# Kernel optimization log

Measured on AMD Instinct MI355X. Metric: run time of the kernel, lower is better.

Reference implementation:

```python
import jax, jax.numpy as jnp
import numpy as np

R_MAX = 6.0
P = 6.0
QQ = 14.399645 * 0.5  # metal units, * 0.5


def setup_inputs() -> dict:
    key = jax.random.key(0)
    k1, k2, k3, k4 = jax.random.split(key, 4)
    n_atoms = 100_000
    n_edges = 6_400_000
    num_types = 4
    # atomic numbers for H, C, O, Cu
    Z = jnp.asarray([1.0, 6.0, 8.0, 29.0], dtype=jnp.float32)
    # edge lengths in (0.1, 7.3) so some edges exceed r_max and get cut off
    r = jax.random.uniform(k1, (n_edges,), dtype=jnp.float32) * 7.2 + 0.1
    per_atom_energy = jax.random.normal(k2, (n_atoms, 1), dtype=jnp.float32)
    atom_types = jax.random.randint(k3, (n_atoms,), 0, num_types, dtype=jnp.int64)
    edge_index = jax.random.randint(k4, (2, n_edges), 0, n_atoms, dtype=jnp.int64)
    return {"Z": Z, "r": r, "per_atom_energy": per_atom_energy,
            "atom_types": atom_types, "edge_index": edge_index}


def _zbl_edge_energy(Z, r, atom_types, edge_index):
    pzbl = 0.23
    a0 = 0.4685
    c1, c2, c3, c4 = 0.02817, 0.28022, 0.50986, 0.18175
    d1, d2, d3, d4 = -0.20162, -0.4029, -0.94229, -3.1998
    edge_types = atom_types[edge_index]          # (2, E)
    Zpair = Z[edge_types]                        # (2, E)
    Zi, Zj = Zpair[0], Zpair[1]
    x = (jnp.power(Zi, pzbl) + jnp.power(Zj, pzbl)) * r / a0
    psi = (c1 * jnp.exp(d1 * x) + c2 * jnp.exp(d2 * x)
           + c3 * jnp.exp(d3 * x) + c4 * jnp.exp(d4 * x))
    eng = QQ * (Zi * Zj / r) * psi
    rr = r / R_MAX
    p = P
    cutoff = (1.0 - (p + 1.0) * (p + 2.0) / 2.0 * jnp.power(rr, p)
              + p * (p + 2.0) * jnp.power(rr, p + 1.0)
              - p * (p + 1.0) / 2.0 * jnp.power(rr, p + 2.0))
    cutoff = cutoff * (rr < 1.0).astype(cutoff.dtype)
    return cutoff * eng                          # (E,)


def reference(Z, r, per_atom_energy, atom_types, edge_index):
    edge_eng = _zbl_edge_energy(Z, r, atom_types, edge_index)
    n_atoms = per_atom_energy.shape[0]
    atomic_eng = jax.ops.segment_sum(edge_eng, edge_index[0],
                                     num_segments=n_atoms)[:, None]
    return atomic_eng + per_atom_energy
```

## Files before the change

kernel.cpp:

```cpp
#include <hip/hip_runtime.h>


namespace {
constexpr float PZBL     = 0.23f;
constexpr float A0_INV   = 1.0f / 0.4685f;
constexpr float C1 = 0.02817f, C2 = 0.28022f, C3 = 0.50986f, C4 = 0.18175f;
constexpr float D1 = -0.20162f, D2 = -0.4029f, D3 = -0.94229f, D4 = -3.1998f;
constexpr float QQ       = 14.399645f * 0.5f;
constexpr float RMAX     = 6.0f;
constexpr float RMAX_INV = 1.0f / 6.0f;
constexpr int   TPW_MAX  = 6400;
constexpr int   P1_BLOCK = 256;
constexpr int   P1_GRID  = 2048;
constexpr int   CHUNK2   = 33344;
constexpr int   BLOCK    = 1024;
constexpr int   S2_MAX   = 86;
constexpr int   CHUNK1   = 25600;
constexpr int   S1_MAX   = 64;
}

__global__ void zbl_pack_types(const int* __restrict__ types,
                               unsigned* __restrict__ tpw,
                               int n_words, int n_atoms) {
    int w = blockIdx.x * blockDim.x + threadIdx.x;
    if (w >= n_words) return;
    unsigned v = 0;
    int base = w * 16;
    int m = min(16, n_atoms - base);
    for (int j = 0; j < m; ++j)
        v |= ((unsigned)types[base + j] & 3u) << (2 * j);
    tpw[w] = v;
}

__device__ __forceinline__ float edge_eng_lds(float rk, int ia, int ib,
                                              const unsigned* s_tp,
                                              const float* s_zz,
                                              const float* s_zx) {
    unsigned ti = (s_tp[ia >> 4] >> ((ia & 15) * 2)) & 3u;
    unsigned tj = (s_tp[ib >> 4] >> ((ib & 15) * 2)) & 3u;
    int tp = (int)((ti << 2) | tj);
    float x = s_zx[tp] * rk;
    float psi = C1 * __expf(D1 * x) + C2 * __expf(D2 * x)
              + C3 * __expf(D3 * x) + C4 * __expf(D4 * x);
    float eng = s_zz[tp] * psi * __builtin_amdgcn_rcpf(rk);
    float rr = rk * RMAX_INV;
    float rr2 = rr * rr;
    float rr3 = rr2 * rr;
    float rr6 = rr3 * rr3;
    float cutoff = 1.0f + rr6 * (-28.0f + rr * (48.0f - 21.0f * rr));
    return (rk < RMAX) ? cutoff * eng : 0.0f;
}

__global__ __launch_bounds__(P1_BLOCK) void zbl_energy_kernel(
    const float*    __restrict__ Z,
    const float*    __restrict__ r,
    const int*      __restrict__ ei0,
    const int*      __restrict__ ei1,
    const unsigned* __restrict__ tpw,
    int4*           __restrict__ rec4,
    int2*           __restrict__ rec2,
    int n_tp_words, int n_quads, int n_edges) {
    __shared__ unsigned s_tp[TPW_MAX];
    __shared__ float    s_zz[16];
    __shared__ float    s_zx[16];

    const int tid = threadIdx.x;
    for (int i = tid; i < n_tp_words; i += P1_BLOCK) s_tp[i] = tpw[i];
    if (tid < 16) {
        int ti = tid >> 2, tj = tid & 3;
        float zi = Z[ti], zj = Z[tj];
        s_zz[tid] = QQ * zi * zj;
        s_zx[tid] = (powf(zi, PZBL) + powf(zj, PZBL)) * A0_INV;
    }
    __syncthreads();

    const float4* r4 = (const float4*)r;
    const int4*   a4 = (const int4*)ei0;
    const int4*   b4 = (const int4*)ei1;
    const int stride = gridDim.x * P1_BLOCK;

    for (int q = blockIdx.x * P1_BLOCK + tid; q < n_quads; q += stride) {
        float4 rv = r4[q];
        int4   av = a4[q];
        int4   bv = b4[q];
        float e0 = edge_eng_lds(rv.x, av.x, bv.x, s_tp, s_zz, s_zx);
        float e1 = edge_eng_lds(rv.y, av.y, bv.y, s_tp, s_zz, s_zx);
        float e2 = edge_eng_lds(rv.z, av.z, bv.z, s_tp, s_zz, s_zx);
        float e3 = edge_eng_lds(rv.w, av.w, bv.w, s_tp, s_zz, s_zx);
        rec4[2 * q]     = make_int4(av.x, __float_as_int(e0),
                                    av.y, __float_as_int(e1));
        rec4[2 * q + 1] = make_int4(av.z, __float_as_int(e2),
                                    av.w, __float_as_int(e3));
    }
    if (blockIdx.x == 0) {
        for (int e = 4 * n_quads + tid; e < n_edges; e += P1_BLOCK) {
            int ia = ei0[e];
            rec2[e] = make_int2(
                ia, __float_as_int(edge_eng_lds(r[e], ia, ei1[e],
                                                s_tp, s_zz, s_zx)));
        }
    }
}

__global__ __launch_bounds__(BLOCK) void zbl_bin_kernel(
    const int4* __restrict__ rec4,
    const int2* __restrict__ rec2,
    float*      __restrict__ partials,
    int n_chunks, int i4_per_slice, int n_i4, int n_records) {
    __shared__ float bins[CHUNK2];
    for (int i = threadIdx.x; i < CHUNK2; i += BLOCK) bins[i] = 0.0f;
    __syncthreads();

    const int c = blockIdx.x % n_chunks;
    const int s = blockIdx.x / n_chunks;
    const int base = c * CHUNK2;

    const int q0 = s * i4_per_slice;
    const int q1 = min(n_i4, q0 + i4_per_slice);
    for (int q = q0 + threadIdx.x; q < q1; q += BLOCK) {
        int4 p = rec4[q];
        unsigned d0 = (unsigned)(p.x - base);
        unsigned d1 = (unsigned)(p.z - base);
        if (d0 < (unsigned)CHUNK2 && p.y != 0)
            atomicAdd(&bins[d0], __int_as_float(p.y));
        if (d1 < (unsigned)CHUNK2 && p.w != 0)
            atomicAdd(&bins[d1], __int_as_float(p.w));
    }
    if (s == 0) {
        for (int e = 2 * n_i4 + threadIdx.x; e < n_records; e += BLOCK) {
            int2 p = rec2[e];
            unsigned d = (unsigned)(p.x - base);
            if (d < (unsigned)CHUNK2 && p.y != 0)
                atomicAdd(&bins[d], __int_as_float(p.y));
        }
    }
    __syncthreads();

    float* dst = partials + (size_t)blockIdx.x * CHUNK2;
    for (int i = threadIdx.x; i < CHUNK2; i += BLOCK) dst[i] = bins[i];
}

__global__ void zbl_reduce_out(const float* __restrict__ pae,
                               const float* __restrict__ partials,
                               float* __restrict__ out,
                               int n_atoms, int n_chunks, int n_slices,
                               int chunk) {
    int a = blockIdx.x * blockDim.x + threadIdx.x;
    if (a >= n_atoms) return;
    int c = a / chunk;
    int i = a - c * chunk;
    const float* p = partials + (size_t)c * chunk + i;
    const size_t stride = (size_t)n_chunks * chunk;
    float s0 = 0.0f, s1 = 0.0f, s2 = 0.0f, s3 = 0.0f;
    int s = 0;
    for (; s + 4 <= n_slices; s += 4) {
        s0 += p[(size_t)(s + 0) * stride];
        s1 += p[(size_t)(s + 1) * stride];
        s2 += p[(size_t)(s + 2) * stride];
        s3 += p[(size_t)(s + 3) * stride];
    }
    for (; s < n_slices; ++s) s0 += p[(size_t)s * stride];
    out[a] = pae[a] + ((s0 + s1) + (s2 + s3));
}

__global__ __launch_bounds__(BLOCK) void zbl_chunk_kernel(
    const float*    __restrict__ Z,
    const float*    __restrict__ r,
    const int*      __restrict__ ei0,
    const int*      __restrict__ ei1,
    const unsigned* __restrict__ tpw,
    float*          __restrict__ partials,
    int n_chunks, int n_tp_words, int quads_per_slice,
    int n_quads, int n_edges) {
    __shared__ float    bins[CHUNK1];
    __shared__ unsigned s_tp[TPW_MAX];
    __shared__ float    s_zz[16];
    __shared__ float    s_zx[16];
    const int tid = threadIdx.x;
    for (int i = tid; i < n_tp_words; i += BLOCK) s_tp[i] = tpw[i];
    if (tid < 16) {
        int ti = tid >> 2, tj = tid & 3;
        float zi = Z[ti], zj = Z[tj];
        s_zz[tid] = QQ * zi * zj;
        s_zx[tid] = (powf(zi, PZBL) + powf(zj, PZBL)) * A0_INV;
    }
    for (int i = tid; i < CHUNK1; i += BLOCK) bins[i] = 0.0f;
    __syncthreads();
    const int c = blockIdx.x % n_chunks;
    const int s = blockIdx.x / n_chunks;
    const int base = c * CHUNK1;
    const int q0 = s * quads_per_slice;
    const int q1 = min(n_quads, q0 + quads_per_slice);
    for (int q = q0 + tid; q < q1; q += BLOCK) {
        int4 av = ((const int4*)ei0)[q];
        unsigned d0 = (unsigned)(av.x - base);
        unsigned d1 = (unsigned)(av.y - base);
        unsigned d2 = (unsigned)(av.z - base);
        unsigned d3 = (unsigned)(av.w - base);
        bool m0 = d0 < (unsigned)CHUNK1, m1 = d1 < (unsigned)CHUNK1;
        bool m2 = d2 < (unsigned)CHUNK1, m3 = d3 < (unsigned)CHUNK1;
        if (!(m0 | m1 | m2 | m3)) continue;
        float4 rv = ((const float4*)r)[q];
        int4   bv = ((const int4*)ei1)[q];
        if (m0) { float e = edge_eng_lds(rv.x, av.x, bv.x, s_tp, s_zz, s_zx);
                  if (e != 0.0f) atomicAdd(&bins[d0], e); }
        if (m1) { float e = edge_eng_lds(rv.y, av.y, bv.y, s_tp, s_zz, s_zx);
                  if (e != 0.0f) atomicAdd(&bins[d1], e); }
        if (m2) { float e = edge_eng_lds(rv.z, av.z, bv.z, s_tp, s_zz, s_zx);
                  if (e != 0.0f) atomicAdd(&bins[d2], e); }
        if (m3) { float e = edge_eng_lds(rv.w, av.w, bv.w, s_tp, s_zz, s_zx);
                  if (e != 0.0f) atomicAdd(&bins[d3], e); }
    }
    if (s == 0) {
        for (int e = 4 * n_quads + tid; e < n_edges; e += BLOCK) {
            int ia = ei0[e];
            unsigned d = (unsigned)(ia - base);
            if (d < (unsigned)CHUNK1) {
                float e2 = edge_eng_lds(r[e], ia, ei1[e], s_tp, s_zz, s_zx);
                if (e2 != 0.0f) atomicAdd(&bins[d], e2);
            }
        }
    }
    __syncthreads();
    float* dst = partials + (size_t)blockIdx.x * CHUNK1;
    for (int i = tid; i < CHUNK1; i += BLOCK) dst[i] = bins[i];
}

__global__ void zbl_init_out(const float* __restrict__ pae,
                             float* __restrict__ out, int n) {
    int i = blockIdx.x * blockDim.x + threadIdx.x;
    if (i < n) out[i] = pae[i];
}

__global__ __launch_bounds__(256) void zbl_edge_fallback(
    const float* __restrict__ Z,
    const float* __restrict__ r,
    const int*   __restrict__ ei0,
    const int*   __restrict__ ei1,
    const int*   __restrict__ types,
    float*       __restrict__ out,
    int n_edges) {
    __shared__ float s_z[4];
    __shared__ float s_zp[4];
    if (threadIdx.x < 4) {
        float z = Z[threadIdx.x];
        s_z[threadIdx.x]  = z;
        s_zp[threadIdx.x] = powf(z, PZBL);
    }
    __syncthreads();
    int e = blockIdx.x * blockDim.x + threadIdx.x;
    if (e >= n_edges) return;
    float rk = r[e];
    if (rk >= RMAX) return;
    int ia = ei0[e], ib = ei1[e];
    int ti = types[ia], tj = types[ib];
    float x = (s_zp[ti] + s_zp[tj]) * rk * A0_INV;
    float psi = C1 * __expf(D1 * x) + C2 * __expf(D2 * x)
              + C3 * __expf(D3 * x) + C4 * __expf(D4 * x);
    float eng = QQ * s_z[ti] * s_z[tj] * psi / rk;
    float rr = rk * RMAX_INV;
    float rr2 = rr * rr, rr3 = rr2 * rr, rr6 = rr3 * rr3;
    float cutoff = 1.0f + rr6 * (-28.0f + rr * (48.0f - 21.0f * rr));
    unsafeAtomicAdd(&out[ia], cutoff * eng);
}

extern "C" void kernel_launch(void* const* d_in, const int* in_sizes, int n_in,
                              void* d_out, int out_size, void* d_ws, size_t ws_size,
                              hipStream_t stream) {
    const float* Z     = (const float*)d_in[0];
    const float* r     = (const float*)d_in[1];
    const float* pae   = (const float*)d_in[2];
    const int*   types = (const int*)d_in[3];
    const int*   ei    = (const int*)d_in[4];

    const int n_edges = in_sizes[1];
    const int n_atoms = in_sizes[2];

    float* out = (float*)d_out;

    const int n_tp_words = (n_atoms + 15) / 16;
    const int n_quads    = (n_edges & 3) ? 0 : (n_edges >> 2);

    const size_t tp_bytes  = ((size_t)n_tp_words * 4 + 15) & ~(size_t)15;
    const size_t rec_bytes = ((size_t)n_edges * 8 + 15) & ~(size_t)15;

    const int nc2 = (n_atoms + CHUNK2 - 1) / CHUNK2;
    int S2 = S2_MAX;
    while (S2 > 4 &&
           tp_bytes + rec_bytes +
           (size_t)nc2 * S2 * CHUNK2 * sizeof(float) > ws_size) {
        --S2;
    }
    const bool two_phase =
        n_tp_words <= TPW_MAX &&
        tp_bytes + rec_bytes + (size_t)nc2 * S2 * CHUNK2 * sizeof(float)
            <= ws_size;

    const int nc1 = (n_atoms + CHUNK1 - 1) / CHUNK1;
    const bool one_phase =
        n_tp_words <= TPW_MAX &&
        tp_bytes + (size_t)nc1 * S1_MAX * CHUNK1 * sizeof(float) <= ws_size;

    if (two_phase) {
        unsigned* tpw = (unsigned*)d_ws;
        int2* rec2 = (int2*)((char*)d_ws + tp_bytes);
        int4* rec4 = (int4*)rec2;
        float* partials = (float*)((char*)d_ws + tp_bytes + rec_bytes);

        zbl_pack_types<<<(n_tp_words + 255) / 256, 256, 0, stream>>>(
            types, tpw, n_tp_words, n_atoms);

        int p1_grid = n_quads ? min(P1_GRID, (n_quads + P1_BLOCK - 1) / P1_BLOCK)
                              : 1;
        zbl_energy_kernel<<<p1_grid, P1_BLOCK, 0, stream>>>(
            Z, r, ei, ei + n_edges, tpw, rec4, rec2,
            n_tp_words, n_quads, n_edges);

        const int n_i4 = n_edges >> 1;
        const int i4_per_slice = (n_i4 + S2 - 1) / S2;
        zbl_bin_kernel<<<nc2 * S2, BLOCK, 0, stream>>>(
            rec4, rec2, partials, nc2, i4_per_slice, n_i4, n_edges);

        zbl_reduce_out<<<(n_atoms + 255) / 256, 256, 0, stream>>>(
            pae, partials, out, n_atoms, nc2, S2, CHUNK2);
    } else if (one_phase) {
        unsigned* tpw = (unsigned*)d_ws;
        float* partials = (float*)((char*)d_ws + tp_bytes);

        zbl_pack_types<<<(n_tp_words + 255) / 256, 256, 0, stream>>>(
            types, tpw, n_tp_words, n_atoms);

        const int quads_per_slice = (n_quads + S1_MAX - 1) / S1_MAX;
        zbl_chunk_kernel<<<nc1 * S1_MAX, BLOCK, 0, stream>>>(
            Z, r, ei, ei + n_edges, tpw, partials,
            nc1, n_tp_words, quads_per_slice, n_quads, n_edges);

        zbl_reduce_out<<<(n_atoms + 255) / 256, 256, 0, stream>>>(
            pae, partials, out, n_atoms, nc1, S1_MAX, CHUNK1);
    } else {
        zbl_init_out<<<(n_atoms + 255) / 256, 256, 0, stream>>>(pae, out, n_atoms);
        zbl_edge_fallback<<<(n_edges + 255) / 256, 256, 0, stream>>>(
            Z, r, ei, ei + n_edges, types, out, n_edges);
    }
}
```

Before: 200.0 us.

## Pack edge records into 32-bit words with truncated bf16 energy

Each edge record now packs the destination atom index (17 bits) with a 15-bit rounded bfloat16 energy into one 32-bit word, halving the intermediate buffer. This aims to cut the write in the energy pass and the repeated reads in the binning pass, where every chunk scans all records. The energy pass processes eight edges per iteration with a fixed grid, and binning loads two uint4 per step with a slice count derived from 256 blocks. The change drops energy precision to bf16 and the sign bit, and restricts the fast path to at most 131072 atoms.

After: 163.3 us. 18.3% less time.

```diff
diff --git a/kernel.cpp b/kernel.cpp
--- a/kernel.cpp
+++ b/kernel.cpp
@@ -11,10 +11,9 @@
 constexpr float RMAX_INV = 1.0f / 6.0f;
 constexpr int   TPW_MAX  = 6400;
 constexpr int   P1_BLOCK = 256;
-constexpr int   P1_GRID  = 2048;
+constexpr int   P1_GRID  = 1536;
 constexpr int   CHUNK2   = 33344;
 constexpr int   BLOCK    = 1024;
-constexpr int   S2_MAX   = 86;
 constexpr int   CHUNK1   = 25600;
 constexpr int   S1_MAX   = 64;
 }
@@ -51,15 +50,20 @@
     return (rk < RMAX) ? cutoff * eng : 0.0f;
 }
 
+__device__ __forceinline__ unsigned pack_rec(int dest, float e) {
+    unsigned b = __float_as_uint(e);
+    unsigned v = (b + 0x8000u) >> 16;
+    return ((unsigned)dest << 15) | (v & 0x7FFFu);
+}
+
 __global__ __launch_bounds__(P1_BLOCK) void zbl_energy_kernel(
     const float*    __restrict__ Z,
     const float*    __restrict__ r,
     const int*      __restrict__ ei0,
     const int*      __restrict__ ei1,
     const unsigned* __restrict__ tpw,
-    int4*           __restrict__ rec4,
-    int2*           __restrict__ rec2,
-    int n_tp_words, int n_quads, int n_edges) {
+    unsigned*       __restrict__ rec,
+    int n_tp_words, int n_oct, int n_edges) {
     __shared__ unsigned s_tp[TPW_MAX];
     __shared__ float    s_zz[16];
     __shared__ float    s_zx[16];
@@ -77,62 +81,66 @@
     const float4* r4 = (const float4*)r;
     const int4*   a4 = (const int4*)ei0;
     const int4*   b4 = (const int4*)ei1;
+    uint4*        rc4 = (uint4*)rec;
     const int stride = gridDim.x * P1_BLOCK;
-
-    for (int q = blockIdx.x * P1_BLOCK + tid; q < n_quads; q += stride) {
-        float4 rv = r4[q];
-        int4   av = a4[q];
-        int4   bv = b4[q];
-        float e0 = edge_eng_lds(rv.x, av.x, bv.x, s_tp, s_zz, s_zx);
-        float e1 = edge_eng_lds(rv.y, av.y, bv.y, s_tp, s_zz, s_zx);
-        float e2 = edge_eng_lds(rv.z, av.z, bv.z, s_tp, s_zz, s_zx);
-        float e3 = edge_eng_lds(rv.w, av.w, bv.w, s_tp, s_zz, s_zx);
-        rec4[2 * q]     = make_int4(av.x, __float_as_int(e0),
-                                    av.y, __float_as_int(e1));
-        rec4[2 * q + 1] = make_int4(av.z, __float_as_int(e2),
-                                    av.w, __float_as_int(e3));
-    }
-    if (blockIdx.x == 0) {
-        for (int e = 4 * n_quads + tid; e < n_edges; e += P1_BLOCK) {
-            int ia = ei0[e];
-            rec2[e] = make_int2(
-                ia, __float_as_int(edge_eng_lds(r[e], ia, ei1[e],
-                                                s_tp, s_zz, s_zx)));
-        }
+    const int gtid = blockIdx.x * P1_BLOCK + tid;
+
+    for (int o = gtid; o < n_oct; o += stride) {
+        int qa = 2 * o, qb = 2 * o + 1;
+        float4 rva = r4[qa], rvb = r4[qb];
+        int4   ava = a4[qa], avb = a4[qb];
+        int4   bva = b4[qa], bvb = b4[qb];
+        uint4 wa, wb;
+        wa.x = pack_rec(ava.x, edge_eng_lds(rva.x, ava.x, bva.x, s_tp, s_zz, s_zx));
+        wa.y = pack_rec(ava.y, edge_eng_lds(rva.y, ava.y, bva.y, s_tp, s_zz, s_zx));
+        wa.z = pack_rec(ava.z, edge_eng_lds(rva.z, ava.z, bva.z, s_tp, s_zz, s_zx));
+        wa.w = pack_rec(ava.w, edge_eng_lds(rva.w, ava.w, bva.w, s_tp, s_zz, s_zx));
+        wb.x = pack_rec(avb.x, edge_eng_lds(rvb.x, avb.x, bvb.x, s_tp, s_zz, s_zx));
+        wb.y = pack_rec(avb.y, edge_eng_lds(rvb.y, avb.y, bvb.y, s_tp, s_zz, s_zx));
+        wb.z = pack_rec(avb.z, edge_eng_lds(rvb.z, avb.z, bvb.z, s_tp, s_zz, s_zx));
+        wb.w = pack_rec(avb.w, edge_eng_lds(rvb.w, avb.w, bvb.w, s_tp, s_zz, s_zx));
+        rc4[qa] = wa;
+        rc4[qb] = wb;
+    }
+    for (int e = 8 * n_oct + gtid; e < n_edges; e += stride) {
+        int ia = ei0[e];
+        rec[e] = pack_rec(ia, edge_eng_lds(r[e], ia, ei1[e], s_tp, s_zz, s_zx));
     }
 }
 
 __global__ __launch_bounds__(BLOCK) void zbl_bin_kernel(
-    const int4* __restrict__ rec4,
-    const int2* __restrict__ rec2,
-    float*      __restrict__ partials,
-    int n_chunks, int i4_per_slice, int n_i4, int n_records) {
+    const uint4* __restrict__ rec4,
+    const unsigned* __restrict__ rec,
+    float*       __restrict__ partials,
+    int n_chunks, int u4_per_slice, int n_u4, int n_records) {
     __shared__ float bins[CHUNK2];
     for (int i = threadIdx.x; i < CHUNK2; i += BLOCK) bins[i] = 0.0f;
     __syncthreads();
 
     const int c = blockIdx.x % n_chunks;
     const int s = blockIdx.x / n_chunks;
-    const int base = c * CHUNK2;
-
-    const int q0 = s * i4_per_slice;
-    const int q1 = min(n_i4, q0 + i4_per_slice);
-    for (int q = q0 + threadIdx.x; q < q1; q += BLOCK) {
-        int4 p = rec4[q];
-        unsigned d0 = (unsigned)(p.x - base);
-        unsigned d1 = (unsigned)(p.z - base);
-        if (d0 < (unsigned)CHUNK2 && p.y != 0)
-            atomicAdd(&bins[d0], __int_as_float(p.y));
-        if (d1 < (unsigned)CHUNK2 && p.w != 0)
-            atomicAdd(&bins[d1], __int_as_float(p.w));
+    const unsigned base = (unsigned)c * CHUNK2;
+
+    auto lane = [&](unsigned w) {
+        unsigned d = (w >> 15) - base;
+        unsigned v = w & 0x7FFFu;
+        if (d < (unsigned)CHUNK2 && v != 0u)
+            atomicAdd(&bins[d], __uint_as_float(v << 16));
+    };
+
+    const int q0 = s * u4_per_slice;
+    const int q1 = min(n_u4, q0 + u4_per_slice);
+    const uint4 dead = make_uint4(0, 0, 0, 0);
+
+    for (int q = q0 + threadIdx.x; q < q1; q += 2 * BLOCK) {
+        uint4 p0 = rec4[q];
+        uint4 p1 = (q + BLOCK < q1) ? rec4[q + BLOCK] : dead;
+        lane(p0.x); lane(p0.y); lane(p0.z); lane(p0.w);
+        lane(p1.x); lane(p1.y); lane(p1.z); lane(p1.w);
     }
     if (s == 0) {
-        for (int e = 2 * n_i4 + threadIdx.x; e < n_records; e += BLOCK) {
-            int2 p = rec2[e];
-            unsigned d = (unsigned)(p.x - base);
-            if (d < (unsigned)CHUNK2 && p.y != 0)
-                atomicAdd(&bins[d], __int_as_float(p.y));
-        }
+        for (int e = 4 * n_u4 + threadIdx.x; e < n_records; e += BLOCK)
+            lane(rec[e]);
     }
     __syncthreads();
 
@@ -282,17 +290,18 @@
     const int n_quads    = (n_edges & 3) ? 0 : (n_edges >> 2);
 
     const size_t tp_bytes  = ((size_t)n_tp_words * 4 + 15) & ~(size_t)15;
-    const size_t rec_bytes = ((size_t)n_edges * 8 + 15) & ~(size_t)15;
+    const size_t rec_bytes = ((size_t)n_edges * 4 + 15) & ~(size_t)15;
 
     const int nc2 = (n_atoms + CHUNK2 - 1) / CHUNK2;
-    int S2 = S2_MAX;
+    int S2 = (nc2 > 0) ? (256 / nc2) : 1;
     while (S2 > 4 &&
            tp_bytes + rec_bytes +
            (size_t)nc2 * S2 * CHUNK2 * sizeof(float) > ws_size) {
         --S2;
     }
     const bool two_phase =
-        n_tp_words <= TPW_MAX &&
+        n_tp_words <= TPW_MAX && n_atoms <= (1 << 17) && S2 >= 4 &&
+        n_quads > 0 &&
         tp_bytes + rec_bytes + (size_t)nc2 * S2 * CHUNK2 * sizeof(float)
             <= ws_size;
 
@@ -303,23 +312,20 @@
 
     if (two_phase) {
         unsigned* tpw = (unsigned*)d_ws;
-        int2* rec2 = (int2*)((char*)d_ws + tp_bytes);
-        int4* rec4 = (int4*)rec2;
+        unsigned* rec = (unsigned*)((char*)d_ws + tp_bytes);
         float* partials = (float*)((char*)d_ws + tp_bytes + rec_bytes);
 
         zbl_pack_types<<<(n_tp_words + 255) / 256, 256, 0, stream>>>(
             types, tpw, n_tp_words, n_atoms);
 
-        int p1_grid = n_quads ? min(P1_GRID, (n_quads + P1_BLOCK - 1) / P1_BLOCK)
-                              : 1;
-        zbl_energy_kernel<<<p1_grid, P1_BLOCK, 0, stream>>>(
-            Z, r, ei, ei + n_edges, tpw, rec4, rec2,
-            n_tp_words, n_quads, n_edges);
-
-        const int n_i4 = n_edges >> 1;
-        const int i4_per_slice = (n_i4 + S2 - 1) / S2;
+        const int n_oct = n_quads >> 1;
+        zbl_energy_kernel<<<P1_GRID, P1_BLOCK, 0, stream>>>(
+            Z, r, ei, ei + n_edges, tpw, rec, n_tp_words, n_oct, n_edges);
+
+        const int n_u4 = n_edges >> 2;
+        const int u4_per_slice = (n_u4 + S2 - 1) / S2;
         zbl_bin_kernel<<<nc2 * S2, BLOCK, 0, stream>>>(
-            rec4, rec2, partials, nc2, i4_per_slice, n_i4, n_edges);
+            (const uint4*)rec, rec, partials, nc2, u4_per_slice, n_u4, n_edges);
 
         zbl_reduce_out<<<(n_atoms + 255) / 256, 256, 0, stream>>>(
             pae, partials, out, n_atoms, nc2, S2, CHUNK2);
```
